# Kernel tuning notes

Measured on AMD Instinct MI355X. Metric: run time of the kernel, lower is better.

## Reference

```python
import jax, jax.numpy as jnp
import numpy as np

NIBBLE_ZERO = 8  # int4 zero-point (symmetric around 8 for unsigned nibble storage)


def _dequant(w_packed, w_scales):
    # w_packed: [out, in//2] int32 holding uint8 bytes, two 4-bit values each.
    low = w_packed & 0xF            # first nibble -> even input positions
    high = (w_packed >> 4) & 0xF    # second nibble -> odd input positions
    out_f = w_packed.shape[0]
    # interleave nibbles along the input dim: [out, in//2, 2] -> [out, in]
    q = jnp.stack([low, high], axis=-1).reshape(out_f, -1)
    return (q.astype(w_scales.dtype) - NIBBLE_ZERO) * w_scales[:, None]  # [out, in]


def setup_inputs() -> dict:
    key = jax.random.key(0)
    k1, k2, k3, k4 = jax.random.split(key, 4)
    N, IN, OUT = 4096, 4096, 4096
    x = jax.random.normal(k1, (N, IN), dtype=jnp.float32)
    w_packed = jax.random.randint(k2, (OUT, IN // 2), 0, 256, dtype=jnp.int32)
    w_scales = jax.random.uniform(k3, (OUT,), dtype=jnp.float32, minval=0.01, maxval=0.05)
    bias = jax.random.normal(k4, (OUT,), dtype=jnp.float32)
    return {"x": x, "w_packed": w_packed, "w_scales": w_scales, "bias": bias}


def reference(x, w_packed, w_scales, bias):
    W = _dequant(w_packed, w_scales)          # [out, in]
    return jnp.einsum('ni,oi->no', x, W) + bias  # [N, out]
```

## Files before the change

kernel.cpp:

```cpp
#include <hip/hip_runtime.h>
#include <hip/hip_bf16.h>


typedef __attribute__((ext_vector_type(8))) __bf16 bf16x8;
typedef __attribute__((ext_vector_type(4))) float f32x4;

#define GLOBAL_AS __attribute__((address_space(1)))
#define LDS_AS __attribute__((address_space(3)))

#define BM 128
#define BN 128
#define BK 64

__device__ inline unsigned short f32_to_bf16(float f) {
    unsigned int u = __float_as_uint(f);
    unsigned int r = (u + 0x7FFFu + ((u >> 16) & 1u)) >> 16;
    return (unsigned short)r;
}

__global__ void prep(const float* __restrict__ x, unsigned short* __restrict__ xb,
                     const int* __restrict__ wp, unsigned short* __restrict__ wb,
                     int n8x, int n4w) {
    const int stride = gridDim.x * blockDim.x;
    const int total = n8x + n4w;
    for (int i = blockIdx.x * blockDim.x + threadIdx.x; i < total; i += stride) {
        if (i < n8x) {
            float4 a = ((const float4*)x)[2 * i];
            float4 b = ((const float4*)x)[2 * i + 1];
            union { unsigned short h[8]; uint4 u; } o;
            o.h[0] = f32_to_bf16(a.x); o.h[1] = f32_to_bf16(a.y);
            o.h[2] = f32_to_bf16(a.z); o.h[3] = f32_to_bf16(a.w);
            o.h[4] = f32_to_bf16(b.x); o.h[5] = f32_to_bf16(b.y);
            o.h[6] = f32_to_bf16(b.z); o.h[7] = f32_to_bf16(b.w);
            ((uint4*)xb)[i] = o.u;
        } else {
            int k = i - n8x;
            int4 v = ((const int4*)wp)[k];
            int vals[4] = {v.x, v.y, v.z, v.w};
            union { unsigned short h[8]; uint4 u; } o;
#pragma unroll
            for (int t = 0; t < 4; ++t) {
                o.h[2 * t]     = f32_to_bf16((float)((vals[t] & 0xF) - 8));
                o.h[2 * t + 1] = f32_to_bf16((float)(((vals[t] >> 4) & 0xF) - 8));
            }
            ((uint4*)wb)[k] = o.u;
        }
    }
}

template<int K, int N>
__global__ __launch_bounds__(256) void gemm_bt(
    const unsigned short* __restrict__ A,
    const unsigned short* __restrict__ B,
    const float* __restrict__ scales,
    const float* __restrict__ bias,
    float* __restrict__ C,
    int GX)
{
    __shared__ unsigned short As[BM * BK];
    __shared__ unsigned short Bs[BN * BK];

    const int tid  = threadIdx.x;
    const int wave = tid >> 6;
    const int lane = tid & 63;
    const int wm = wave >> 1;
    const int wn = wave & 1;

    const int bid = blockIdx.x;
    const int g   = bid >> 3;
    const int t8  = bid & 7;
    const int sgx = GX >> 2;
    const int bx  = (g % sgx) * 4 + (t8 & 3);
    const int by  = (g / sgx) * 2 + (t8 >> 2);
    const int m0 = by * BM;
    const int n0 = bx * BN;

    f32x4 acc[4][4];
#pragma unroll
    for (int i = 0; i < 4; ++i)
#pragma unroll
        for (int j = 0; j < 4; ++j)
            acc[i][j] = (f32x4){0.f, 0.f, 0.f, 0.f};

    const int srow = tid >> 3;
    const int scol = ((tid & 7) ^ (srow & 7)) * 8;

    const unsigned short* Ag = A + (size_t)(m0 + srow) * K + scol;
    const unsigned short* Bg = B + (size_t)(n0 + srow) * K + scol;

    const int am = lane & 15;
    const int aq = lane >> 4;
    const int cbyte = ((aq ^ (am & 7)) << 4);

    int aoffB[4], boffB[4];
#pragma unroll
    for (int i = 0; i < 4; ++i)
        aoffB[i] = (wm * 64 + i * 16 + am) * (BK * 2) + cbyte;
#pragma unroll
    for (int j = 0; j < 4; ++j)
        boffB[j] = (wn * 64 + j * 16 + am) * (BK * 2) + cbyte;

    const char* AsB = (const char*)As;
    const char* BsB = (const char*)Bs;

    for (int k0 = 0; k0 < K; k0 += BK) {
#pragma unroll
        for (int j = 0; j < 4; ++j) {
            __builtin_amdgcn_global_load_lds(
                (const GLOBAL_AS void*)(Ag + (size_t)(j * 32) * K + k0),
                (LDS_AS void*)(As + tid * 8 + j * 2048), 16, 0, 0);
        }
#pragma unroll
        for (int j = 0; j < 4; ++j) {
            __builtin_amdgcn_global_load_lds(
                (const GLOBAL_AS void*)(Bg + (size_t)(j * 32) * K + k0),
                (LDS_AS void*)(Bs + tid * 8 + j * 2048), 16, 0, 0);
        }
        __syncthreads();

        {
            bf16x8 af[4], bfr[4];
#pragma unroll
            for (int i = 0; i < 4; ++i) af[i] = *(const bf16x8*)(AsB + aoffB[i]);
#pragma unroll
            for (int j = 0; j < 4; ++j) bfr[j] = *(const bf16x8*)(BsB + boffB[j]);
#pragma unroll
            for (int i = 0; i < 4; ++i)
#pragma unroll
                for (int j = 0; j < 4; ++j)
                    acc[i][j] = __builtin_amdgcn_mfma_f32_16x16x32_bf16(af[i], bfr[j], acc[i][j], 0, 0, 0);
        }
        {
            bf16x8 af[4], bfr[4];
#pragma unroll
            for (int i = 0; i < 4; ++i) af[i] = *(const bf16x8*)(AsB + (aoffB[i] ^ 64));
#pragma unroll
            for (int j = 0; j < 4; ++j) bfr[j] = *(const bf16x8*)(BsB + (boffB[j] ^ 64));
#pragma unroll
            for (int i = 0; i < 4; ++i)
#pragma unroll
                for (int j = 0; j < 4; ++j)
                    acc[i][j] = __builtin_amdgcn_mfma_f32_16x16x32_bf16(af[i], bfr[j], acc[i][j], 0, 0, 0);
        }
        __syncthreads();
    }

    const int cq = lane >> 4;
    const int cc = lane & 15;
#pragma unroll
    for (int j = 0; j < 4; ++j) {
        const int col = n0 + wn * 64 + j * 16 + cc;
        const float s = scales[col];
        const float b = bias[col];
#pragma unroll
        for (int i = 0; i < 4; ++i) {
            const int rowb = m0 + wm * 64 + i * 16 + cq * 4;
#pragma unroll
            for (int r = 0; r < 4; ++r) {
                C[(size_t)(rowb + r) * N + col] = acc[i][j][r] * s + b;
            }
        }
    }
}

__global__ void naive_kernel(const float* __restrict__ x, const int* __restrict__ wp,
                             const float* __restrict__ sc, const float* __restrict__ bs,
                             float* __restrict__ out, int NR, int OUTF, int INF) {
    int idx = blockIdx.x * 256 + threadIdx.x;
    if (idx >= NR * OUTF) return;
    int n = idx / OUTF, o = idx - n * OUTF;
    const float* xr = x + (size_t)n * INF;
    const int* wr = wp + (size_t)o * (INF / 2);
    float acc = 0.f;
    for (int c = 0; c < INF / 2; ++c) {
        int v = wr[c];
        acc += xr[2 * c] * (float)((v & 0xF) - 8) + xr[2 * c + 1] * (float)(((v >> 4) & 0xF) - 8);
    }
    out[idx] = acc * sc[o] + bs[o];
}

extern "C" void kernel_launch(void* const* d_in, const int* in_sizes, int n_in,
                              void* d_out, int out_size, void* d_ws, size_t ws_size,
                              hipStream_t stream) {
    const float* x      = (const float*)d_in[0];
    const int*   wp     = (const int*)d_in[1];
    const float* scales = (const float*)d_in[2];
    const float* bias   = (const float*)d_in[3];
    float* out = (float*)d_out;

    const int OUTF = in_sizes[2];
    const int INF  = (2 * in_sizes[1]) / OUTF;
    const int NR   = in_sizes[0] / INF;

    unsigned short* xb = (unsigned short*)d_ws;
    unsigned short* wb = xb + (size_t)NR * INF;
    const size_t need = ((size_t)NR * INF + (size_t)OUTF * INF) * sizeof(unsigned short);

    if (ws_size >= need && INF == 4096 && OUTF == 4096 && (NR % BM) == 0
        && (in_sizes[0] % 8) == 0 && (in_sizes[1] % 4) == 0) {
        prep<<<2048, 256, 0, stream>>>(x, xb, wp, wb, in_sizes[0] / 8, in_sizes[1] / 4);
        const int GX = OUTF / BN;
        const int GY = NR / BM;
        gemm_bt<4096, 4096><<<GX * GY, 256, 0, stream>>>(xb, wb, scales, bias, out, GX);
    } else {
        int total = NR * OUTF;
        naive_kernel<<<(total + 255) / 256, 256, 0, stream>>>(x, wp, scales, bias, out, NR, OUTF, INF);
    }
}
```

Baseline: 291.1 us.

## Use 256x256 tiles with double-buffered LDS and interleaved load/MFMA pipeline

Rewrites the bf16 GEMM to use 256x256 block tiles with 512 threads (8 waves) and a 128KB double-buffered LDS ring. Global-to-LDS loads for the next k-steps are issued in quarter chunks between MFMA groups, with explicit barriers, waitcnt and setprio, so memory traffic overlaps compute. Block ids are remapped into an XCD-chunked order for cache locality. This cuts per-FLOP global traffic and sync stalls, at the cost of higher register pressure, 1 block/CU occupancy, and fragile hand-tuned synchronization.

```diff
diff --git a/kernel.cpp b/kernel.cpp
--- a/kernel.cpp
+++ b/kernel.cpp
@@ -8,8 +8,8 @@
 #define GLOBAL_AS __attribute__((address_space(1)))
 #define LDS_AS __attribute__((address_space(3)))
 
-#define BM 128
-#define BN 128
+#define BM 256
+#define BN 256
 #define BK 64
 
 __device__ inline unsigned short f32_to_bf16(float f) {
@@ -49,118 +49,170 @@
 }
 
 template<int K, int N>
-__global__ __launch_bounds__(256) void gemm_bt(
+__global__ __launch_bounds__(512, 2) void gemm_bt(
     const unsigned short* __restrict__ A,
     const unsigned short* __restrict__ B,
     const float* __restrict__ scales,
     const float* __restrict__ bias,
     float* __restrict__ C,
-    int GX)
+    int GY)
 {
-    __shared__ unsigned short As[BM * BK];
-    __shared__ unsigned short Bs[BN * BK];
+    constexpr int NT = K / BK;
+    __shared__ __align__(16) unsigned short lds[65536];
 
     const int tid  = threadIdx.x;
     const int wave = tid >> 6;
     const int lane = tid & 63;
-    const int wm = wave >> 1;
-    const int wn = wave & 1;
+    const int wm = wave >> 2;
+    const int wn = wave & 3;
 
     const int bid = blockIdx.x;
-    const int g   = bid >> 3;
-    const int t8  = bid & 7;
-    const int sgx = GX >> 2;
-    const int bx  = (g % sgx) * 4 + (t8 & 3);
-    const int by  = (g / sgx) * 2 + (t8 >> 2);
+    const int chunk = gridDim.x >> 3;
+    const int sw = (bid & 7) * chunk + (bid >> 3);
+    const int bx = sw / GY;
+    const int by = sw - bx * GY;
     const int m0 = by * BM;
     const int n0 = bx * BN;
 
-    f32x4 acc[4][4];
-#pragma unroll
-    for (int i = 0; i < 4; ++i)
+    const int am = lane & 15;
+    const int aq = lane >> 4;
+    const int cb = ((aq ^ (am & 7)) << 4);
+
+    int aoff[8], boff[4];
+#pragma unroll
+    for (int i = 0; i < 8; ++i) {
+        int r = (2 * i + wm) * 16 + am;
+        aoff[i] = ((i < 4) ? 0 : 16384) + (r & 127) * 128 + cb;
+    }
+#pragma unroll
+    for (int j = 0; j < 4; ++j) {
+        int r = (4 * j + wn) * 16 + am;
+        boff[j] = 32768 + ((j < 2) ? 0 : 16384) + (r & 127) * 128 + cb;
+    }
+
+    const int sch = tid & 7;
+    const int r0 = tid >> 3;
+    const int r1 = (512 + tid) >> 3;
+    const size_t g0 = (size_t)r0 * K + (size_t)((sch ^ (r0 & 7)) * 8);
+    const size_t g1 = (size_t)r1 * K + (size_t)((sch ^ (r1 & 7)) * 8);
+    const int d0 = tid * 8;
+    const int d1 = (512 + tid) * 8;
+
+    const unsigned short* Abase = A + (size_t)m0 * K;
+    const unsigned short* Bbase = B + (size_t)n0 * K;
+
+    f32x4 acc[8][4];
+#pragma unroll
+    for (int i = 0; i < 8; ++i)
 #pragma unroll
         for (int j = 0; j < 4; ++j)
             acc[i][j] = (f32x4){0.f, 0.f, 0.f, 0.f};
 
-    const int srow = tid >> 3;
-    const int scol = ((tid & 7) ^ (srow & 7)) * 8;
-
-    const unsigned short* Ag = A + (size_t)(m0 + srow) * K + scol;
-    const unsigned short* Bg = B + (size_t)(n0 + srow) * K + scol;
-
-    const int am = lane & 15;
-    const int aq = lane >> 4;
-    const int cbyte = ((aq ^ (am & 7)) << 4);
-
-    int aoffB[4], boffB[4];
-#pragma unroll
-    for (int i = 0; i < 4; ++i)
-        aoffB[i] = (wm * 64 + i * 16 + am) * (BK * 2) + cbyte;
-#pragma unroll
-    for (int j = 0; j < 4; ++j)
-        boffB[j] = (wn * 64 + j * 16 + am) * (BK * 2) + cbyte;
-
-    const char* AsB = (const char*)As;
-    const char* BsB = (const char*)Bs;
-
-    for (int k0 = 0; k0 < K; k0 += BK) {
-#pragma unroll
-        for (int j = 0; j < 4; ++j) {
-            __builtin_amdgcn_global_load_lds(
-                (const GLOBAL_AS void*)(Ag + (size_t)(j * 32) * K + k0),
-                (LDS_AS void*)(As + tid * 8 + j * 2048), 16, 0, 0);
-        }
-#pragma unroll
-        for (int j = 0; j < 4; ++j) {
-            __builtin_amdgcn_global_load_lds(
-                (const GLOBAL_AS void*)(Bg + (size_t)(j * 32) * K + k0),
-                (LDS_AS void*)(Bs + tid * 8 + j * 2048), 16, 0, 0);
-        }
-        __syncthreads();
-
-        {
-            bf16x8 af[4], bfr[4];
-#pragma unroll
-            for (int i = 0; i < 4; ++i) af[i] = *(const bf16x8*)(AsB + aoffB[i]);
-#pragma unroll
-            for (int j = 0; j < 4; ++j) bfr[j] = *(const bf16x8*)(BsB + boffB[j]);
-#pragma unroll
-            for (int i = 0; i < 4; ++i)
-#pragma unroll
-                for (int j = 0; j < 4; ++j)
-                    acc[i][j] = __builtin_amdgcn_mfma_f32_16x16x32_bf16(af[i], bfr[j], acc[i][j], 0, 0, 0);
-        }
-        {
-            bf16x8 af[4], bfr[4];
-#pragma unroll
-            for (int i = 0; i < 4; ++i) af[i] = *(const bf16x8*)(AsB + (aoffB[i] ^ 64));
-#pragma unroll
-            for (int j = 0; j < 4; ++j) bfr[j] = *(const bf16x8*)(BsB + (boffB[j] ^ 64));
-#pragma unroll
-            for (int i = 0; i < 4; ++i)
-#pragma unroll
-                for (int j = 0; j < 4; ++j)
-                    acc[i][j] = __builtin_amdgcn_mfma_f32_16x16x32_bf16(af[i], bfr[j], acc[i][j], 0, 0, 0);
-        }
-        __syncthreads();
+    const char* ldsB = (const char*)lds;
+    bf16x8 af[4][2], bf[2][2];
+
+#define STAGE(gbase, half, kcol, uoff)                                            \
+    do {                                                                          \
+        const unsigned short* _g = (gbase) + (size_t)((half) * 128) * K + (kcol); \
+        __builtin_amdgcn_global_load_lds((const GLOBAL_AS void*)(_g + g0),        \
+            (LDS_AS void*)(lds + (uoff) + d0), 16, 0, 0);                         \
+        __builtin_amdgcn_global_load_lds((const GLOBAL_AS void*)(_g + g1),        \
+            (LDS_AS void*)(lds + (uoff) + d1), 16, 0, 0);                         \
+    } while (0)
+
+#define LDA(mh, OB)                                                               \
+    _Pragma("unroll") for (int i2 = 0; i2 < 4; ++i2) {                            \
+        af[i2][0] = *(const bf16x8*)(ldsB + (OB) + aoff[(mh) * 4 + i2]);          \
+        af[i2][1] = *(const bf16x8*)(ldsB + (OB) + (aoff[(mh) * 4 + i2] ^ 64));   \
+    }
+
+#define LDB(nh, OB)                                                               \
+    _Pragma("unroll") for (int j2 = 0; j2 < 2; ++j2) {                            \
+        bf[j2][0] = *(const bf16x8*)(ldsB + (OB) + boff[(nh) * 2 + j2]);          \
+        bf[j2][1] = *(const bf16x8*)(ldsB + (OB) + (boff[(nh) * 2 + j2] ^ 64));   \
+    }
+
+#define BAR_LG()                                                                  \
+    __builtin_amdgcn_s_barrier();                                                 \
+    asm volatile("s_waitcnt lgkmcnt(0)" ::: "memory");                            \
+    __builtin_amdgcn_sched_barrier(0)
+
+#define MFMA_Q(mh, nh)                                                            \
+    _Pragma("unroll") for (int i2 = 0; i2 < 4; ++i2)                              \
+    _Pragma("unroll") for (int j2 = 0; j2 < 2; ++j2) {                            \
+        acc[(mh) * 4 + i2][(nh) * 2 + j2] = __builtin_amdgcn_mfma_f32_16x16x32_bf16( \
+            af[i2][0], bf[j2][0], acc[(mh) * 4 + i2][(nh) * 2 + j2], 0, 0, 0);    \
+        acc[(mh) * 4 + i2][(nh) * 2 + j2] = __builtin_amdgcn_mfma_f32_16x16x32_bf16( \
+            af[i2][1], bf[j2][1], acc[(mh) * 4 + i2][(nh) * 2 + j2], 0, 0, 0);    \
+    }
+
+#define GROUP(OB, OUS, OUSo, t)                                                   \
+    {                                                                             \
+        const int kn1 = (((t) + 1 < NT) ? (t) + 1 : NT - 1) * BK;                 \
+        const int kn2 = (((t) + 2 < NT) ? (t) + 2 : NT - 1) * BK;                 \
+                                                             \
+        LDA(0, OB); LDB(0, OB);                                                   \
+        STAGE(Bbase, 0, kn1, (OUSo) + 16384);                                     \
+        BAR_LG();                                                                 \
+        __builtin_amdgcn_s_setprio(1); MFMA_Q(0, 0); __builtin_amdgcn_s_setprio(0); \
+        __builtin_amdgcn_s_barrier();                                             \
+                                                             \
+        LDB(1, OB);                                                               \
+        STAGE(Abase, 1, kn1, (OUSo) + 8192);                                      \
+        BAR_LG();                                                                 \
+        __builtin_amdgcn_s_setprio(1); MFMA_Q(0, 1); __builtin_amdgcn_s_setprio(0); \
+        __builtin_amdgcn_s_barrier();                                             \
+                                                             \
+        LDA(1, OB);                                                               \
+        STAGE(Abase, 0, kn2, (OUS) + 0);                                          \
+        BAR_LG();                                                                 \
+        __builtin_amdgcn_s_setprio(1); MFMA_Q(1, 1); __builtin_amdgcn_s_setprio(0); \
+        __builtin_amdgcn_s_barrier();                                             \
+                                                             \
+        LDB(0, OB);                                                               \
+        STAGE(Bbase, 1, kn2, (OUS) + 24576);                                      \
+        asm volatile("s_waitcnt vmcnt(4)" ::: "memory");                          \
+        BAR_LG();                                                                 \
+        __builtin_amdgcn_s_setprio(1); MFMA_Q(1, 0); __builtin_amdgcn_s_setprio(0); \
+        __builtin_amdgcn_s_barrier();                                             \
+    }
+
+    STAGE(Abase, 0, 0, 0);
+    STAGE(Bbase, 1, 0, 24576);
+    STAGE(Bbase, 0, 0, 16384);
+    STAGE(Abase, 1, 0, 8192);
+    STAGE(Abase, 0, BK, 32768);
+    STAGE(Bbase, 1, BK, 32768 + 24576);
+    asm volatile("s_waitcnt vmcnt(4)" ::: "memory");
+    __builtin_amdgcn_s_barrier();
+
+    for (int t = 0; t < NT; t += 2) {
+        GROUP(0, 0, 32768, t);
+        GROUP(65536, 32768, 0, t + 1);
     }
 
     const int cq = lane >> 4;
     const int cc = lane & 15;
 #pragma unroll
     for (int j = 0; j < 4; ++j) {
-        const int col = n0 + wn * 64 + j * 16 + cc;
+        const int col = n0 + (4 * j + wn) * 16 + cc;
         const float s = scales[col];
         const float b = bias[col];
 #pragma unroll
-        for (int i = 0; i < 4; ++i) {
-            const int rowb = m0 + wm * 64 + i * 16 + cq * 4;
+        for (int i = 0; i < 8; ++i) {
+            const int rowb = m0 + (2 * i + wm) * 16 + cq * 4;
 #pragma unroll
             for (int r = 0; r < 4; ++r) {
                 C[(size_t)(rowb + r) * N + col] = acc[i][j][r] * s + b;
             }
         }
     }
+#undef STAGE
+#undef LDA
+#undef LDB
+#undef BAR_LG
+#undef MFMA_Q
+#undef GROUP
 }
 
 __global__ void naive_kernel(const float* __restrict__ x, const int* __restrict__ wp,
@@ -196,12 +248,14 @@
     unsigned short* wb = xb + (size_t)NR * INF;
     const size_t need = ((size_t)NR * INF + (size_t)OUTF * INF) * sizeof(unsigned short);
 
+    const int GX = OUTF / BN;
+    const int GY = NR / BM;
+
     if (ws_size >= need && INF == 4096 && OUTF == 4096 && (NR % BM) == 0
+        && ((GX * GY) % 8) == 0
         && (in_sizes[0] % 8) == 0 && (in_sizes[1] % 4) == 0) {
         prep<<<2048, 256, 0, stream>>>(x, xb, wp, wb, in_sizes[0] / 8, in_sizes[1] / 4);
-        const int GX = OUTF / BN;
-        const int GY = NR / BM;
-        gemm_bt<4096, 4096><<<GX * GY, 256, 0, stream>>>(xb, wb, scales, bias, out, GX);
+        gemm_bt<4096, 4096><<<GX * GY, 512, 0, stream>>>(xb, wb, scales, bias, out, GY);
     } else {
         int total = NR * OUTF;
         naive_kernel<<<(total + 255) / 256, 256, 0, stream>>>(x, wp, scales, bias, out, NR, OUTF, INF);
```

Result: faster. 264.1 us (-9.3%).
